# Kernel optimization log

Measured on AMD Instinct MI355X. Metric: run time of the kernel, lower is better.

The kernel has to match this reference:

```python
import jax, jax.numpy as jnp
import numpy as np

R_GUIDED = 81      # guided filter radius (kernel 163x163)
EPS = 1e-3
W_COEF = 0.95
MAXV1 = 0.8
BINS = 2000
MINFILT_R = 7      # min-filter radius (kernel 15x15)
NEG_BIG = -1.0e30


def box_mean(x, r):
    # avg_pool2d(kernel=2r+1, stride=1, padding=r, count_include_pad=True)
    # via O(1)-per-pixel integral image. x: [B,H,W]
    k = 2 * r + 1
    xp = jnp.pad(x, ((0, 0), (r, r), (r, r)))
    S = jnp.cumsum(jnp.cumsum(xp, axis=1), axis=2)
    S = jnp.pad(S, ((0, 0), (1, 0), (1, 0)))
    box = S[:, k:, k:] - S[:, :-k, k:] - S[:, k:, :-k] + S[:, :-k, :-k]
    return box / float(k * k)


def min_filter(x, r):
    # -max_pool2d(-x, kernel=2r+1, stride=1, padding=r); torch pads max-pool with -inf
    if r <= 0:
        return x
    k = 2 * r + 1
    return -jax.lax.reduce_window(-x, -jnp.inf, jax.lax.max,
                                  (1, k, k), (1, 1, 1),
                                  [(0, 0), (r, r), (r, r)])


def guided_filter(I, p, r, eps):
    I_mean = box_mean(I, r)
    p_mean = box_mean(p, r)
    Ip_mean = box_mean(I * p, r)
    I_var = box_mean(I * I, r) - I_mean * I_mean
    cov_Ip = Ip_mean - I_mean * p_mean
    a = cov_Ip / (I_var + eps)
    b = p_mean - a * I_mean
    return box_mean(a, r) * I + box_mean(b, r)


def setup_inputs() -> dict:
    key = jax.random.key(0)
    x = jax.random.uniform(key, (8, 3, 768, 1024), dtype=jnp.float32)
    return {"x": x}


def reference(x):
    m = x * 255.0                      # [B,3,H,W]
    V1 = jnp.min(m, axis=1)            # dark channel, [B,H,W]
    V1 = guided_filter(V1, min_filter(V1, MINFILT_R), R_GUIDED, EPS)

    # torch.histc(V1, bins=2000): range [min, max], max value falls in last bin
    mn = jnp.min(V1)
    mx = jnp.max(V1)
    idx = jnp.clip(((V1 - mn) / (mx - mn) * BINS).astype(jnp.int32), 0, BINS - 1)
    hist = jnp.zeros((BINS,), V1.dtype).at[idx.reshape(-1)].add(1.0)
    d = jnp.cumsum(hist) / float(V1.size)
    lmax = jnp.max(jnp.where(d <= 0.999, jnp.arange(BINS), -1))
    thresh = hist[lmax]                # faithful to original: a COUNT used as threshold

    m_mean_c = jnp.mean(m, axis=1)     # [B,H,W]
    mask = V1 >= thresh
    A_cand = jnp.max(jnp.where(mask, m_mean_c, NEG_BIG))
    A_fallback = jnp.max(jnp.mean(m, axis=(1, 2, 3)))
    A = jnp.where(jnp.any(mask), A_cand, A_fallback)

    V1c = jnp.minimum(V1 * W_COEF, MAXV1)           # clamp(max=maxV1)
    Y = (m - V1c[:, None]) / (1.0 - V1c[:, None] / A)
    return jnp.clip(Y, 0.0, 1.0)
```

## Files before the change

### kernel.cpp

```cpp
#include <hip/hip_runtime.h>

#define BATCH 8
#define HH 768
#define WW 1024
#define HW (HH*WW)
#define NPIX (BATCH*HW)
#define RG 81
#define KG (2*RG+1)
#define INVK2 (1.0f/((float)KG*(float)KG))
#define RM 7
#define EPSF 1e-3f
#define NBINS 2000
#define NEG_BIG_F (-1.0e30f)
#define NROWS (BATCH*HH)

#define CHV 48
#define NCHV (HH/CHV)
#define CHM 32
#define NCHM (HH/CHM)


__device__ inline unsigned fkey(float f) {
    unsigned u = __float_as_uint(f);
    return (u & 0x80000000u) ? ~u : (u | 0x80000000u);
}
__device__ inline float funkey(unsigned k) {
    unsigned u = (k & 0x80000000u) ? (k & 0x7fffffffu) : ~k;
    return __uint_as_float(u);
}

__device__ inline void f2add(float2& a, const float2& b) { a.x += b.x; a.y += b.y; }
__device__ inline void f2sub(float2& a, const float2& b) { a.x -= b.x; a.y -= b.y; }

__device__ inline float waveInclScan(float x) {
    int lane = threadIdx.x & 63;
#pragma unroll
    for (int d = 1; d < 64; d <<= 1) {
        float u = __shfl_up(x, (unsigned)d, 64);
        if (lane >= d) x += u;
    }
    return x;
}

__device__ inline void scanRow(float v0, float v1, float v2, float v3,
                               float* cum, float* wsum) {
    int tid = threadIdx.x;
    float c0 = v0, c1 = c0 + v1, c2 = c1 + v2, c3 = c2 + v3;
    float inc = waveInclScan(c3);
    int lane = tid & 63, wv = tid >> 6;
    if (lane == 63) wsum[wv] = inc;
    __syncthreads();
    float basev = 0.f;
    if (wv > 0) basev += wsum[0];
    if (wv > 1) basev += wsum[1];
    if (wv > 2) basev += wsum[2];
    float ex = basev + inc - c3;
    cum[4 * tid + 0] = ex + c0;
    cum[4 * tid + 1] = ex + c1;
    cum[4 * tid + 2] = ex + c2;
    cum[4 * tid + 3] = ex + c3;
}


__global__ void k_init(unsigned* scal, unsigned* hist) {
    int t = threadIdx.x;
    for (int i = t; i < NBINS; i += 256) hist[i] = 0u;
    if (t == 0) {
        scal[0] = 0xFFFFFFFFu;
        scal[1] = 0u;
        scal[2] = 0u;
        scal[3] = 0u;
    }
}

__global__ __launch_bounds__(256) void k_prep(const float* __restrict__ x,
                                              float* __restrict__ V1raw,
                                              float* __restrict__ mmean,
                                              float* __restrict__ hmin,
                                              float* __restrict__ pbsum) {
    int img = blockIdx.x / HH;
    int row = blockIdx.x % HH;
    int pix = row * WW + threadIdx.x * 4;
    size_t base = (size_t)img * 3 * HW + pix;
    float4 c0 = *(const float4*)(x + base);
    float4 c1 = *(const float4*)(x + base + HW);
    float4 c2 = *(const float4*)(x + base + 2 * (size_t)HW);
    float4 mnv, mev;
    {
        float a0 = c0.x * 255.0f, a1 = c1.x * 255.0f, a2 = c2.x * 255.0f;
        mnv.x = fminf(a0, fminf(a1, a2)); mev.x = (a0 + a1 + a2) * (1.0f / 3.0f);
        a0 = c0.y * 255.0f; a1 = c1.y * 255.0f; a2 = c2.y * 255.0f;
        mnv.y = fminf(a0, fminf(a1, a2)); mev.y = (a0 + a1 + a2) * (1.0f / 3.0f);
        a0 = c0.z * 255.0f; a1 = c1.z * 255.0f; a2 = c2.z * 255.0f;
        mnv.z = fminf(a0, fminf(a1, a2)); mev.z = (a0 + a1 + a2) * (1.0f / 3.0f);
        a0 = c0.w * 255.0f; a1 = c1.w * 255.0f; a2 = c2.w * 255.0f;
        mnv.w = fminf(a0, fminf(a1, a2)); mev.w = (a0 + a1 + a2) * (1.0f / 3.0f);
    }
    size_t po = (size_t)img * HW + pix;
    *(float4*)(V1raw + po) = mnv;
    *(float4*)(mmean + po) = mev;

    __shared__ float r[WW];
    int t = threadIdx.x;
    r[4 * t + 0] = mnv.x; r[4 * t + 1] = mnv.y; r[4 * t + 2] = mnv.z; r[4 * t + 3] = mnv.w;

    float s = mev.x + mev.y + mev.z + mev.w;
#pragma unroll
    for (int d = 32; d >= 1; d >>= 1) s += __shfl_down(s, (unsigned)d, 64);
    __shared__ float wsum[4];
    int lane = t & 63, wv = t >> 6;
    if (lane == 0) wsum[wv] = s;
    __syncthreads();
    if (t == 0)
        pbsum[blockIdx.x] = wsum[0] + wsum[1] + wsum[2] + wsum[3];

    float v[18];
#pragma unroll
    for (int i = 0; i < 18; i++) {
        int w = 4 * t - RM + i;
        w = w < 0 ? 0 : (w > WW - 1 ? WW - 1 : w);
        v[i] = r[w];
    }
#pragma unroll
    for (int i = 0; i < 17; i++) v[i] = fminf(v[i], v[i + 1]);
#pragma unroll
    for (int i = 0; i < 15; i++) v[i] = fminf(v[i], v[i + 2]);
#pragma unroll
    for (int i = 0; i < 11; i++) v[i] = fminf(v[i], v[i + 4]);
    float4 o;
    o.x = fminf(v[0], v[7]);
    o.y = fminf(v[1], v[8]);
    o.z = fminf(v[2], v[9]);
    o.w = fminf(v[3], v[10]);
    *(float4*)(hmin + po) = o;
}

__global__ __launch_bounds__(256) void k_imgsum(const float* __restrict__ pbsum,
                                                double* __restrict__ imgsum) {
    int img = blockIdx.x;
    const float* p = pbsum + img * HH;
    double s = 0.0;
    for (int i = threadIdx.x; i < HH; i += 256) s += (double)p[i];
#pragma unroll
    for (int d = 32; d >= 1; d >>= 1) s += __shfl_down(s, (unsigned)d, 64);
    __shared__ double wsum[4];
    int lane = threadIdx.x & 63, wv = threadIdx.x >> 6;
    if (lane == 0) wsum[wv] = s;
    __syncthreads();
    if (threadIdx.x == 0)
        imgsum[img] = wsum[0] + wsum[1] + wsum[2] + wsum[3];
}

__global__ __launch_bounds__(256) void k_minv(const float* __restrict__ in,
                                              float* __restrict__ out) {
    int g = blockIdx.x * 256 + threadIdx.x;
    int w = g & (WW - 1);
    int t = g >> 10;
    int b = t / NCHM;
    int ch = t - b * NCHM;
    int h0 = ch * CHM;
    const float* col = in + (size_t)b * HW + w;
    float* ocol = out + (size_t)b * HW + w;
    float v[CHM + 14];
#pragma unroll
    for (int i = 0; i < CHM + 14; i++) {
        int h = h0 - RM + i;
        h = h < 0 ? 0 : (h > HH - 1 ? HH - 1 : h);
        v[i] = col[(size_t)h * WW];
    }
#pragma unroll
    for (int i = 0; i < CHM + 13; i++) v[i] = fminf(v[i], v[i + 1]);
#pragma unroll
    for (int i = 0; i < CHM + 11; i++) v[i] = fminf(v[i], v[i + 2]);
#pragma unroll
    for (int i = 0; i < CHM + 7; i++)  v[i] = fminf(v[i], v[i + 4]);
#pragma unroll
    for (int i = 0; i < CHM; i++)
        ocol[(size_t)(h0 + i) * WW] = fminf(v[i], v[i + 7]);
}

__global__ __launch_bounds__(256) void k_kv1(const float* __restrict__ I,
                                             const float* __restrict__ p,
                                             float4* __restrict__ F4) {
    int g = blockIdx.x * 256 + threadIdx.x;
    int w = g & (WW - 1);
    int t = g >> 10;
    int b = t / NCHV;
    int ch = t - b * NCHV;
    int h0 = ch * CHV;
    const float* colI = I + (size_t)b * HW + w;
    const float* colP = p + (size_t)b * HW + w;
    float4* out = F4 + (size_t)b * HW + w;

    int jlo = h0 - RG; if (jlo < 0) jlo = 0;
    int jhi = h0 + RG - 1; if (jhi > HH - 1) jhi = HH - 1;
    float sI = 0.f, sP = 0.f, sIp = 0.f, sII = 0.f;
    float Li[8], Lp[8];
    int j = jlo;
    for (; j + 7 <= jhi; j += 8) {
#pragma unroll
        for (int k = 0; k < 8; k++) { Li[k] = colI[(size_t)(j + k) * WW]; Lp[k] = colP[(size_t)(j + k) * WW]; }
#pragma unroll
        for (int k = 0; k < 8; k++) { sI += Li[k]; sP += Lp[k]; sIp += Li[k] * Lp[k]; sII += Li[k] * Li[k]; }
    }
    for (; j <= jhi; j++) {
        float a = colI[(size_t)j * WW], c = colP[(size_t)j * WW];
        sI += a; sP += c; sIp += a * c; sII += a * a;
    }

    if (h0 >= RG + 1 && h0 + CHV - 1 + RG <= HH - 1) {
        float Ai[8], Ap[8], Si[8], Sp[8];
        for (int h = h0; h < h0 + CHV; h += 8) {
#pragma unroll
            for (int k = 0; k < 8; k++) { Ai[k] = colI[(size_t)(h + RG + k) * WW]; Ap[k] = colP[(size_t)(h + RG + k) * WW]; }
#pragma unroll
            for (int k = 0; k < 8; k++) { Si[k] = colI[(size_t)(h - RG + k) * WW]; Sp[k] = colP[(size_t)(h - RG + k) * WW]; }
#pragma unroll
            for (int k = 0; k < 8; k++) {
                sI += Ai[k]; sP += Ap[k]; sIp += Ai[k] * Ap[k]; sII += Ai[k] * Ai[k];
                out[(size_t)(h + k) * WW] = make_float4(sI, sP, sIp, sII);
                sI -= Si[k]; sP -= Sp[k]; sIp -= Si[k] * Sp[k]; sII -= Si[k] * Si[k];
            }
        }
    } else {
        for (int h = h0; h < h0 + CHV; h++) {
            if (h + RG <= HH - 1) {
                float a = colI[(size_t)(h + RG) * WW], c = colP[(size_t)(h + RG) * WW];
                sI += a; sP += c; sIp += a * c; sII += a * a;
            }
            out[(size_t)h * WW] = make_float4(sI, sP, sIp, sII);
            if (h - RG >= 0) {
                float a = colI[(size_t)(h - RG) * WW], c = colP[(size_t)(h - RG) * WW];
                sI -= a; sP -= c; sIp -= a * c; sII -= a * a;
            }
        }
    }
}

__global__ __launch_bounds__(256) void k_kh1(const float4* __restrict__ F4,
                                             float2* __restrict__ AB) {
    __shared__ float cI[WW], cP[WW], cIp[WW], cII[WW];
    __shared__ float w0[4], w1[4], w2[4], w3[4];
    size_t base = (size_t)blockIdx.x * WW;
    int t = threadIdx.x;
    float4 q0 = F4[base + 4 * t + 0];
    float4 q1 = F4[base + 4 * t + 1];
    float4 q2 = F4[base + 4 * t + 2];
    float4 q3 = F4[base + 4 * t + 3];
    scanRow(q0.x, q1.x, q2.x, q3.x, cI, w0);
    scanRow(q0.y, q1.y, q2.y, q3.y, cP, w1);
    scanRow(q0.z, q1.z, q2.z, q3.z, cIp, w2);
    scanRow(q0.w, q1.w, q2.w, q3.w, cII, w3);
    __syncthreads();
    float oa[4], ob[4];
#pragma unroll
    for (int j = 0; j < 4; j++) {
        int w = 4 * t + j;
        int hi = w + RG; if (hi > WW - 1) hi = WW - 1;
        int lo = w - RG - 1;
        float a = cI[hi], b = cP[hi], c = cIp[hi], d = cII[hi];
        if (lo >= 0) { a -= cI[lo]; b -= cP[lo]; c -= cIp[lo]; d -= cII[lo]; }
        float mI = a * INVK2, mP = b * INVK2, mIp = c * INVK2, mII = d * INVK2;
        float av = (mIp - mI * mP) / ((mII - mI * mI) + EPSF);
        oa[j] = av; ob[j] = mP - av * mI;
    }
    ((float4*)(AB + base))[2 * t]     = make_float4(oa[0], ob[0], oa[1], ob[1]);
    ((float4*)(AB + base))[2 * t + 1] = make_float4(oa[2], ob[2], oa[3], ob[3]);
}

__global__ __launch_bounds__(256) void k_kv2(const float2* __restrict__ AB,
                                             float2* __restrict__ SAB) {
    int g = blockIdx.x * 256 + threadIdx.x;
    int w = g & (WW - 1);
    int t = g >> 10;
    int b = t / NCHV;
    int ch = t - b * NCHV;
    int h0 = ch * CHV;
    const float2* col = AB + (size_t)b * HW + w;
    float2* out = SAB + (size_t)b * HW + w;

    int jlo = h0 - RG; if (jlo < 0) jlo = 0;
    int jhi = h0 + RG - 1; if (jhi > HH - 1) jhi = HH - 1;
    float2 s0 = {0,0}, s1 = {0,0}, s2 = {0,0}, s3 = {0,0};
    float2 L[8];
    int j = jlo;
    for (; j + 7 <= jhi; j += 8) {
#pragma unroll
        for (int k = 0; k < 8; k++) L[k] = col[(size_t)(j + k) * WW];
        f2add(s0, L[0]); f2add(s1, L[1]); f2add(s2, L[2]); f2add(s3, L[3]);
        f2add(s0, L[4]); f2add(s1, L[5]); f2add(s2, L[6]); f2add(s3, L[7]);
    }
    for (; j <= jhi; j++) f2add(s0, col[(size_t)j * WW]);
    f2add(s0, s1); f2add(s2, s3); f2add(s0, s2);
    float2 acc = s0;

    if (h0 >= RG + 1 && h0 + CHV - 1 + RG <= HH - 1) {
        float2 A[8], S[8];
        for (int h = h0; h < h0 + CHV; h += 8) {
#pragma unroll
            for (int k = 0; k < 8; k++) A[k] = col[(size_t)(h + RG + k) * WW];
#pragma unroll
            for (int k = 0; k < 8; k++) S[k] = col[(size_t)(h - RG + k) * WW];
#pragma unroll
            for (int k = 0; k < 8; k++) {
                f2add(acc, A[k]);
                out[(size_t)(h + k) * WW] = acc;
                f2sub(acc, S[k]);
            }
        }
    } else {
        for (int h = h0; h < h0 + CHV; h++) {
            if (h + RG <= HH - 1) f2add(acc, col[(size_t)(h + RG) * WW]);
            out[(size_t)h * WW] = acc;
            if (h - RG >= 0) f2sub(acc, col[(size_t)(h - RG) * WW]);
        }
    }
}

__global__ __launch_bounds__(256) void k_kh2(const float2* __restrict__ SAB,
                                             const float* __restrict__ I,
                                             float* __restrict__ V1,
                                             float* __restrict__ bmin,
                                             float* __restrict__ bmax) {
    __shared__ float cA[WW], cB[WW];
    __shared__ float w0[4], w1[4];
    size_t base = (size_t)blockIdx.x * WW;
    int t = threadIdx.x;
    float4 q0 = ((const float4*)(SAB + base))[2 * t];
    float4 q1 = ((const float4*)(SAB + base))[2 * t + 1];
    scanRow(q0.x, q0.z, q1.x, q1.z, cA, w0);
    scanRow(q0.y, q0.w, q1.y, q1.w, cB, w1);
    __syncthreads();
    float4 iv = ((const float4*)(I + base))[t];
    float Ij[4] = {iv.x, iv.y, iv.z, iv.w};
    float ov[4];
    float lmn = 3.4e38f, lmx = -3.4e38f;
#pragma unroll
    for (int j = 0; j < 4; j++) {
        int w = 4 * t + j;
        int hi = w + RG; if (hi > WW - 1) hi = WW - 1;
        int lo = w - RG - 1;
        float a = cA[hi], b = cB[hi];
        if (lo >= 0) { a -= cA[lo]; b -= cB[lo]; }
        float v = a * INVK2 * Ij[j] + b * INVK2;
        ov[j] = v;
        lmn = fminf(lmn, v); lmx = fmaxf(lmx, v);
    }
    ((float4*)(V1 + base))[t] = make_float4(ov[0], ov[1], ov[2], ov[3]);
#pragma unroll
    for (int d = 32; d >= 1; d >>= 1) {
        lmn = fminf(lmn, __shfl_down(lmn, (unsigned)d, 64));
        lmx = fmaxf(lmx, __shfl_down(lmx, (unsigned)d, 64));
    }
    __shared__ float smn[4], smx[4];
    int lane = t & 63, wv = t >> 6;
    if (lane == 0) { smn[wv] = lmn; smx[wv] = lmx; }
    __syncthreads();
    if (t == 0) {
        bmin[blockIdx.x] = fminf(fminf(smn[0], smn[1]), fminf(smn[2], smn[3]));
        bmax[blockIdx.x] = fmaxf(fmaxf(smx[0], smx[1]), fmaxf(smx[2], smx[3]));
    }
}

__global__ __launch_bounds__(256) void k_mm(const float* __restrict__ bmin,
                                            const float* __restrict__ bmax,
                                            unsigned* __restrict__ scal) {
    float mn = 3.4e38f, mx = -3.4e38f;
    for (int i = threadIdx.x; i < NROWS; i += 256) {
        mn = fminf(mn, bmin[i]);
        mx = fmaxf(mx, bmax[i]);
    }
#pragma unroll
    for (int d = 32; d >= 1; d >>= 1) {
        mn = fminf(mn, __shfl_down(mn, (unsigned)d, 64));
        mx = fmaxf(mx, __shfl_down(mx, (unsigned)d, 64));
    }
    __shared__ float smn[4], smx[4];
    int lane = threadIdx.x & 63, wv = threadIdx.x >> 6;
    if (lane == 0) { smn[wv] = mn; smx[wv] = mx; }
    __syncthreads();
    if (threadIdx.x == 0) {
        float a = fminf(fminf(smn[0], smn[1]), fminf(smn[2], smn[3]));
        float b = fmaxf(fmaxf(smx[0], smx[1]), fmaxf(smx[2], smx[3]));
        scal[0] = fkey(a);
        scal[1] = fkey(b);
    }
}

__global__ __launch_bounds__(256) void k_hist(const float* __restrict__ V1,
                                              const unsigned* __restrict__ scal,
                                              unsigned* __restrict__ hist) {
    __shared__ unsigned lh[NBINS];
    for (int i = threadIdx.x; i < NBINS; i += 256) lh[i] = 0u;
    __syncthreads();
    float mn = funkey(scal[0]);
    float mx = funkey(scal[1]);
    float inv = 2000.0f / (mx - mn);
    const float4* V4 = (const float4*)V1;
    for (int i = blockIdx.x * 256 + threadIdx.x; i < NPIX / 4; i += gridDim.x * 256) {
        float4 v = V4[i];
        int i0 = (int)((v.x - mn) * inv); i0 = i0 < 0 ? 0 : (i0 > NBINS - 1 ? NBINS - 1 : i0);
        int i1 = (int)((v.y - mn) * inv); i1 = i1 < 0 ? 0 : (i1 > NBINS - 1 ? NBINS - 1 : i1);
        int i2 = (int)((v.z - mn) * inv); i2 = i2 < 0 ? 0 : (i2 > NBINS - 1 ? NBINS - 1 : i2);
        int i3 = (int)((v.w - mn) * inv); i3 = i3 < 0 ? 0 : (i3 > NBINS - 1 ? NBINS - 1 : i3);
        atomicAdd(&lh[i0], 1u);
        atomicAdd(&lh[i1], 1u);
        atomicAdd(&lh[i2], 1u);
        atomicAdd(&lh[i3], 1u);
    }
    __syncthreads();
    for (int i = threadIdx.x; i < NBINS; i += 256) {
        unsigned c = lh[i];
        if (c) atomicAdd(&hist[i], c);
    }
}

__global__ __launch_bounds__(256) void k_thresh(const unsigned* __restrict__ hist,
                                                float* __restrict__ fscal) {
    int t = threadIdx.x;
    unsigned h[8];
    float local = 0.f;
#pragma unroll
    for (int j = 0; j < 8; j++) {
        int idx = t * 8 + j;
        h[j] = (idx < NBINS) ? hist[idx] : 0u;
        local += (float)h[j];
    }
    float inc = waveInclScan(local);
    __shared__ float wsum[4];
    __shared__ int smax[4];
    int lane = t & 63, wv = t >> 6;
    if (lane == 63) wsum[wv] = inc;
    __syncthreads();
    float basev = 0.f;
    if (wv > 0) basev += wsum[0];
    if (wv > 1) basev += wsum[1];
    if (wv > 2) basev += wsum[2];
    float cum = basev + inc - local;
    int lmax = -1;
#pragma unroll
    for (int j = 0; j < 8; j++) {
        int idx = t * 8 + j;
        cum += (float)h[j];
        float d = cum / (float)NPIX;
        if (idx < NBINS && d <= 0.999f) lmax = idx;
    }
#pragma unroll
    for (int d = 32; d >= 1; d >>= 1) {
        int o = __shfl_down(lmax, (unsigned)d, 64);
        lmax = o > lmax ? o : lmax;
    }
    if (lane == 0) smax[wv] = lmax;
    __syncthreads();
    if (t == 0) {
        int m = smax[0];
        if (smax[1] > m) m = smax[1];
        if (smax[2] > m) m = smax[2];
        if (smax[3] > m) m = smax[3];
        int idx = m < 0 ? NBINS - 1 : m;
        fscal[4] = (float)hist[idx];
    }
}

__global__ __launch_bounds__(256) void k_amax(const float* __restrict__ V1,
                                              const float* __restrict__ mmean,
                                              const float* __restrict__ fscal,
                                              unsigned* __restrict__ scal) {
    float th = fscal[4];
    float lmax = NEG_BIG_F;
    bool any = false;
    const float4* V4 = (const float4*)V1;
    const float4* M4 = (const float4*)mmean;
    for (int i = blockIdx.x * 256 + threadIdx.x; i < NPIX / 4; i += gridDim.x * 256) {
        float4 v = V4[i];
        if (v.x >= th || v.y >= th || v.z >= th || v.w >= th) {
            float4 m = M4[i];
            any = true;
            if (v.x >= th) lmax = fmaxf(lmax, m.x);
            if (v.y >= th) lmax = fmaxf(lmax, m.y);
            if (v.z >= th) lmax = fmaxf(lmax, m.z);
            if (v.w >= th) lmax = fmaxf(lmax, m.w);
        }
    }
#pragma unroll
    for (int d = 32; d >= 1; d >>= 1) lmax = fmaxf(lmax, __shfl_down(lmax, (unsigned)d, 64));
    unsigned long long ab = __ballot(any);
    __shared__ float smx[4];
    __shared__ unsigned sany[4];
    int lane = threadIdx.x & 63, wv = threadIdx.x >> 6;
    if (lane == 0) { smx[wv] = lmax; sany[wv] = ab ? 1u : 0u; }
    __syncthreads();
    if (threadIdx.x == 0) {
        float m = fmaxf(fmaxf(smx[0], smx[1]), fmaxf(smx[2], smx[3]));
        unsigned a = sany[0] | sany[1] | sany[2] | sany[3];
        if (a) {
            atomicOr(&scal[3], 1u);
            atomicMax(&scal[2], fkey(m));
        }
    }
}

__global__ void k_selA(const unsigned* __restrict__ scal,
                       const double* __restrict__ imgsum,
                       float* __restrict__ fscal) {
    if (threadIdx.x != 0 || blockIdx.x != 0) return;
    float A;
    if (scal[3]) {
        A = funkey(scal[2]);
    } else {
        double best = -1e300;
        for (int b = 0; b < BATCH; b++) {
            double m = imgsum[b] / (double)HW;
            if (m > best) best = m;
        }
        A = (float)best;
    }
    fscal[5] = A;
}

__global__ __launch_bounds__(256) void k_final(const float* __restrict__ x,
                                               const float* __restrict__ V1,
                                               const float* __restrict__ fscal,
                                               float* __restrict__ out) {
    float A = fscal[5];
    float invA = 1.0f / A;
    int i = (blockIdx.x * 256 + threadIdx.x) * 4;
    int b = i / HW;
    int pix = i - b * HW;
    float4 v1 = *(const float4*)(V1 + i);
    float4 v1c, den;
    v1c.x = fminf(v1.x * 0.95f, 0.8f); den.x = 1.0f / (1.0f - v1c.x * invA);
    v1c.y = fminf(v1.y * 0.95f, 0.8f); den.y = 1.0f / (1.0f - v1c.y * invA);
    v1c.z = fminf(v1.z * 0.95f, 0.8f); den.z = 1.0f / (1.0f - v1c.z * invA);
    v1c.w = fminf(v1.w * 0.95f, 0.8f); den.w = 1.0f / (1.0f - v1c.w * invA);
    size_t o = (size_t)b * 3 * HW + pix;
#pragma unroll
    for (int c = 0; c < 3; c++) {
        float4 m = *(const float4*)(x + o);
        float4 y;
        y.x = fminf(fmaxf((m.x * 255.0f - v1c.x) * den.x, 0.0f), 1.0f);
        y.y = fminf(fmaxf((m.y * 255.0f - v1c.y) * den.y, 0.0f), 1.0f);
        y.z = fminf(fmaxf((m.z * 255.0f - v1c.z) * den.z, 0.0f), 1.0f);
        y.w = fminf(fmaxf((m.w * 255.0f - v1c.w) * den.w, 0.0f), 1.0f);
        *(float4*)(out + o) = y;
        o += HW;
    }
}


extern "C" void kernel_launch(void* const* d_in, const int* in_sizes, int n_in,
                              void* d_out, int out_size, void* d_ws, size_t ws_size,
                              hipStream_t stream) {
    const float* x = (const float*)d_in[0];
    float* out = (float*)d_out;

    unsigned* scal = (unsigned*)d_ws;
    float* fscal = (float*)d_ws;
    double* imgsum = (double*)((char*)d_ws + 32);
    unsigned* hist = (unsigned*)((char*)d_ws + 96);
    float* pbsum = (float*)((char*)d_ws + 8192);
    float* bmin  = (float*)((char*)d_ws + 32768);
    float* bmax  = (float*)((char*)d_ws + 57344);
    float* planes = (float*)((char*)d_ws + 131072);
    float* P0 = planes + (size_t)0 * NPIX;
    float* P1 = planes + (size_t)1 * NPIX;
    float* P2 = planes + (size_t)2 * NPIX;
    float* P3 = planes + (size_t)3 * NPIX;
    float* P6 = planes + (size_t)6 * NPIX;
    float4* F4 = (float4*)(planes + (size_t)4 * NPIX);
    float2* AB = (float2*)P2;
    float2* SAB = (float2*)(planes + (size_t)4 * NPIX);

    k_init<<<1, 256, 0, stream>>>(scal, hist);
    k_prep<<<NROWS, 256, 0, stream>>>(x, P0, P1, P2, pbsum);
    k_imgsum<<<BATCH, 256, 0, stream>>>(pbsum, imgsum);
    k_minv<<<BATCH * NCHM * WW / 256, 256, 0, stream>>>(P2, P3);
    k_kv1<<<BATCH * NCHV * WW / 256, 256, 0, stream>>>(P0, P3, F4);
    k_kh1<<<NROWS, 256, 0, stream>>>(F4, AB);
    k_kv2<<<BATCH * NCHV * WW / 256, 256, 0, stream>>>(AB, SAB);
    k_kh2<<<NROWS, 256, 0, stream>>>(SAB, P0, P6, bmin, bmax);
    k_mm<<<1, 256, 0, stream>>>(bmin, bmax, scal);
    k_hist<<<1024, 256, 0, stream>>>(P6, scal, hist);
    k_thresh<<<1, 256, 0, stream>>>(hist, fscal);
    k_amax<<<1024, 256, 0, stream>>>(P6, P1, fscal, scal);
    k_selA<<<1, 64, 0, stream>>>(scal, imgsum, fscal);
    k_final<<<NPIX / 1024, 256, 0, stream>>>(x, P6, fscal, out);
}
```

Baseline: 276.5 us.

## Fuse second horizontal box pass into kh1 and final combine into kv2

The second box filter of a and b is reordered so the horizontal prefix-sum pass runs inside k_kh1, right after a and b are computed in shared memory. The vertical pass then produces V1 directly, along with the per-block min/max. This drops the k_kh2 kernel and one full read and write of the float2 SAB plane. k_kv2 now also reads the I plane, and k_mm reduces NVB block partials instead of per-row partials.

```diff
diff --git a/kernel.cpp b/kernel.cpp
--- a/kernel.cpp
+++ b/kernel.cpp
@@ -16,6 +16,7 @@
 
 #define CHV 48
 #define NCHV (HH/CHV)
+#define NVB (BATCH*NCHV*(WW/256))
 #define CHM 32
 #define NCHM (HH/CHM)
 
@@ -238,9 +239,10 @@
 }
 
 __global__ __launch_bounds__(256) void k_kh1(const float4* __restrict__ F4,
-                                             float2* __restrict__ AB) {
+                                             float2* __restrict__ HAB) {
     __shared__ float cI[WW], cP[WW], cIp[WW], cII[WW];
-    __shared__ float w0[4], w1[4], w2[4], w3[4];
+    __shared__ float cA[WW], cB[WW];
+    __shared__ float w0[4], w1[4], w2[4], w3[4], w4[4], w5[4];
     size_t base = (size_t)blockIdx.x * WW;
     int t = threadIdx.x;
     float4 q0 = F4[base + 4 * t + 0];
@@ -252,7 +254,7 @@
     scanRow(q0.z, q1.z, q2.z, q3.z, cIp, w2);
     scanRow(q0.w, q1.w, q2.w, q3.w, cII, w3);
     __syncthreads();
-    float oa[4], ob[4];
+    float av[4], bv[4];
 #pragma unroll
     for (int j = 0; j < 4; j++) {
         int w = 4 * t + j;
@@ -261,23 +263,41 @@
         float a = cI[hi], b = cP[hi], c = cIp[hi], d = cII[hi];
         if (lo >= 0) { a -= cI[lo]; b -= cP[lo]; c -= cIp[lo]; d -= cII[lo]; }
         float mI = a * INVK2, mP = b * INVK2, mIp = c * INVK2, mII = d * INVK2;
-        float av = (mIp - mI * mP) / ((mII - mI * mI) + EPSF);
-        oa[j] = av; ob[j] = mP - av * mI;
-    }
-    ((float4*)(AB + base))[2 * t]     = make_float4(oa[0], ob[0], oa[1], ob[1]);
-    ((float4*)(AB + base))[2 * t + 1] = make_float4(oa[2], ob[2], oa[3], ob[3]);
-}
-
-__global__ __launch_bounds__(256) void k_kv2(const float2* __restrict__ AB,
-                                             float2* __restrict__ SAB) {
+        float aa = (mIp - mI * mP) / ((mII - mI * mI) + EPSF);
+        av[j] = aa; bv[j] = mP - aa * mI;
+    }
+    __syncthreads();
+    scanRow(av[0], av[1], av[2], av[3], cA, w4);
+    scanRow(bv[0], bv[1], bv[2], bv[3], cB, w5);
+    __syncthreads();
+    float oa[4], ob[4];
+#pragma unroll
+    for (int j = 0; j < 4; j++) {
+        int w = 4 * t + j;
+        int hi = w + RG; if (hi > WW - 1) hi = WW - 1;
+        int lo = w - RG - 1;
+        float a = cA[hi], b = cB[hi];
+        if (lo >= 0) { a -= cA[lo]; b -= cB[lo]; }
+        oa[j] = a; ob[j] = b;
+    }
+    ((float4*)(HAB + base))[2 * t]     = make_float4(oa[0], ob[0], oa[1], ob[1]);
+    ((float4*)(HAB + base))[2 * t + 1] = make_float4(oa[2], ob[2], oa[3], ob[3]);
+}
+
+__global__ __launch_bounds__(256) void k_kv2(const float2* __restrict__ HAB,
+                                             const float* __restrict__ I,
+                                             float* __restrict__ V1,
+                                             float* __restrict__ bmin,
+                                             float* __restrict__ bmax) {
     int g = blockIdx.x * 256 + threadIdx.x;
     int w = g & (WW - 1);
     int t = g >> 10;
     int b = t / NCHV;
     int ch = t - b * NCHV;
     int h0 = ch * CHV;
-    const float2* col = AB + (size_t)b * HW + w;
-    float2* out = SAB + (size_t)b * HW + w;
+    const float2* col = HAB + (size_t)b * HW + w;
+    const float* icol = I + (size_t)b * HW + w;
+    float* vcol = V1 + (size_t)b * HW + w;
 
     int jlo = h0 - RG; if (jlo < 0) jlo = 0;
     int jhi = h0 + RG - 1; if (jhi > HH - 1) jhi = HH - 1;
@@ -294,69 +314,45 @@
     f2add(s0, s1); f2add(s2, s3); f2add(s0, s2);
     float2 acc = s0;
 
+    float lmn = 3.4e38f, lmx = -3.4e38f;
     if (h0 >= RG + 1 && h0 + CHV - 1 + RG <= HH - 1) {
         float2 A[8], S[8];
+        float Iv[8];
         for (int h = h0; h < h0 + CHV; h += 8) {
 #pragma unroll
             for (int k = 0; k < 8; k++) A[k] = col[(size_t)(h + RG + k) * WW];
 #pragma unroll
             for (int k = 0; k < 8; k++) S[k] = col[(size_t)(h - RG + k) * WW];
+#pragma unroll
+            for (int k = 0; k < 8; k++) Iv[k] = icol[(size_t)(h + k) * WW];
 #pragma unroll
             for (int k = 0; k < 8; k++) {
                 f2add(acc, A[k]);
-                out[(size_t)(h + k) * WW] = acc;
+                float v = acc.x * INVK2 * Iv[k] + acc.y * INVK2;
+                vcol[(size_t)(h + k) * WW] = v;
+                lmn = fminf(lmn, v); lmx = fmaxf(lmx, v);
                 f2sub(acc, S[k]);
             }
         }
     } else {
         for (int h = h0; h < h0 + CHV; h++) {
             if (h + RG <= HH - 1) f2add(acc, col[(size_t)(h + RG) * WW]);
-            out[(size_t)h * WW] = acc;
+            float v = acc.x * INVK2 * icol[(size_t)h * WW] + acc.y * INVK2;
+            vcol[(size_t)h * WW] = v;
+            lmn = fminf(lmn, v); lmx = fmaxf(lmx, v);
             if (h - RG >= 0) f2sub(acc, col[(size_t)(h - RG) * WW]);
         }
     }
-}
-
-__global__ __launch_bounds__(256) void k_kh2(const float2* __restrict__ SAB,
-                                             const float* __restrict__ I,
-                                             float* __restrict__ V1,
-                                             float* __restrict__ bmin,
-                                             float* __restrict__ bmax) {
-    __shared__ float cA[WW], cB[WW];
-    __shared__ float w0[4], w1[4];
-    size_t base = (size_t)blockIdx.x * WW;
-    int t = threadIdx.x;
-    float4 q0 = ((const float4*)(SAB + base))[2 * t];
-    float4 q1 = ((const float4*)(SAB + base))[2 * t + 1];
-    scanRow(q0.x, q0.z, q1.x, q1.z, cA, w0);
-    scanRow(q0.y, q0.w, q1.y, q1.w, cB, w1);
-    __syncthreads();
-    float4 iv = ((const float4*)(I + base))[t];
-    float Ij[4] = {iv.x, iv.y, iv.z, iv.w};
-    float ov[4];
-    float lmn = 3.4e38f, lmx = -3.4e38f;
-#pragma unroll
-    for (int j = 0; j < 4; j++) {
-        int w = 4 * t + j;
-        int hi = w + RG; if (hi > WW - 1) hi = WW - 1;
-        int lo = w - RG - 1;
-        float a = cA[hi], b = cB[hi];
-        if (lo >= 0) { a -= cA[lo]; b -= cB[lo]; }
-        float v = a * INVK2 * Ij[j] + b * INVK2;
-        ov[j] = v;
-        lmn = fminf(lmn, v); lmx = fmaxf(lmx, v);
-    }
-    ((float4*)(V1 + base))[t] = make_float4(ov[0], ov[1], ov[2], ov[3]);
 #pragma unroll
     for (int d = 32; d >= 1; d >>= 1) {
         lmn = fminf(lmn, __shfl_down(lmn, (unsigned)d, 64));
         lmx = fmaxf(lmx, __shfl_down(lmx, (unsigned)d, 64));
     }
     __shared__ float smn[4], smx[4];
-    int lane = t & 63, wv = t >> 6;
+    int lane = threadIdx.x & 63, wv = threadIdx.x >> 6;
     if (lane == 0) { smn[wv] = lmn; smx[wv] = lmx; }
     __syncthreads();
-    if (t == 0) {
+    if (threadIdx.x == 0) {
         bmin[blockIdx.x] = fminf(fminf(smn[0], smn[1]), fminf(smn[2], smn[3]));
         bmax[blockIdx.x] = fmaxf(fmaxf(smx[0], smx[1]), fmaxf(smx[2], smx[3]));
     }
@@ -366,7 +362,7 @@
                                             const float* __restrict__ bmax,
                                             unsigned* __restrict__ scal) {
     float mn = 3.4e38f, mx = -3.4e38f;
-    for (int i = threadIdx.x; i < NROWS; i += 256) {
+    for (int i = threadIdx.x; i < NVB; i += 256) {
         mn = fminf(mn, bmin[i]);
         mx = fmaxf(mx, bmax[i]);
     }
@@ -568,17 +564,15 @@
     float* P3 = planes + (size_t)3 * NPIX;
     float* P6 = planes + (size_t)6 * NPIX;
     float4* F4 = (float4*)(planes + (size_t)4 * NPIX);
-    float2* AB = (float2*)P2;
-    float2* SAB = (float2*)(planes + (size_t)4 * NPIX);
+    float2* HAB = (float2*)P2;
 
     k_init<<<1, 256, 0, stream>>>(scal, hist);
     k_prep<<<NROWS, 256, 0, stream>>>(x, P0, P1, P2, pbsum);
     k_imgsum<<<BATCH, 256, 0, stream>>>(pbsum, imgsum);
     k_minv<<<BATCH * NCHM * WW / 256, 256, 0, stream>>>(P2, P3);
     k_kv1<<<BATCH * NCHV * WW / 256, 256, 0, stream>>>(P0, P3, F4);
-    k_kh1<<<NROWS, 256, 0, stream>>>(F4, AB);
-    k_kv2<<<BATCH * NCHV * WW / 256, 256, 0, stream>>>(AB, SAB);
-    k_kh2<<<NROWS, 256, 0, stream>>>(SAB, P0, P6, bmin, bmax);
+    k_kh1<<<NROWS, 256, 0, stream>>>(F4, HAB);
+    k_kv2<<<NVB, 256, 0, stream>>>(HAB, P0, P6, bmin, bmax);
     k_mm<<<1, 256, 0, stream>>>(bmin, bmax, scal);
     k_hist<<<1024, 256, 0, stream>>>(P6, scal, hist);
     k_thresh<<<1, 256, 0, stream>>>(hist, fscal);
```

Result: faster. 269.1 us (-2.7%).
